# Kernel optimization log

Hardware: AMD Instinct MI355X
Metric: run time of the kernel (lower is better)

## Reference

```python
import jax, jax.numpy as jnp
import numpy as np

SEQ, B, H, OUT = 128, 256, 1024, 128


def _linear_params(key, out_dim, in_dim):
    kw, kb = jax.random.split(key)
    bound = 1.0 / np.sqrt(in_dim)
    W = jax.random.uniform(kw, (out_dim, in_dim), jnp.float32, -bound, bound)
    b = jax.random.uniform(kb, (out_dim,), jnp.float32, -bound, bound)
    return W, b


def setup_inputs() -> dict:
    key = jax.random.key(0)
    keys = jax.random.split(key, 10)
    x = jax.random.normal(keys[0], (SEQ, B), jnp.float32)
    Wfx, bfx = _linear_params(keys[1], H, 1)
    Wfh, bfh = _linear_params(keys[2], H, H)
    Wix, bix = _linear_params(keys[3], H, 1)
    Wih, bih = _linear_params(keys[4], H, H)
    Wgx, bgx = _linear_params(keys[5], H, 1)
    Wgh, bgh = _linear_params(keys[6], H, H)
    Wox, box = _linear_params(keys[7], H, 1)
    Woh, boh = _linear_params(keys[8], H, H)
    Wph, bph = _linear_params(keys[9], OUT, H)
    return dict(x=x, Wfx=Wfx, bfx=bfx, Wfh=Wfh, bfh=bfh,
                Wix=Wix, bix=bix, Wih=Wih, bih=bih,
                Wgx=Wgx, bgx=bgx, Wgh=Wgh, bgh=bgh,
                Wox=Wox, box=box, Woh=Woh, boh=boh,
                Wph=Wph, bph=bph)


def reference(x, Wfx, bfx, Wfh, bfh, Wix, bix, Wih, bih,
              Wgx, bgx, Wgh, bgh, Wox, box, Woh, boh, Wph, bph):
    # Fuse the 8 per-gate linears into two GEMMs per step (x-proj and h-proj),
    # gate order: f, i, g, o.
    Wx = jnp.concatenate([Wfx, Wix, Wgx, Wox], axis=0)      # (4H, 1)
    bx = jnp.concatenate([bfx, bix, bgx, box], axis=0)       # (4H,)
    Wh = jnp.concatenate([Wfh, Wih, Wgh, Woh], axis=0)       # (4H, H)
    bh = jnp.concatenate([bfh, bih, bgh, boh], axis=0)       # (4H,)
    Hdim = Wfh.shape[0]
    Bsz = x.shape[1]

    # x projection has input_dim=1: precompute for all timesteps at once.
    zx_all = x[:, :, None] * Wx[:, 0][None, None, :] + bx     # (S, B, 4H)

    def step(carry, zx):
        h, c = carry
        z = zx + h @ Wh.T + bh                                # (B, 4H)
        f = jax.nn.sigmoid(z[:, 0 * Hdim:1 * Hdim])
        i = jax.nn.sigmoid(z[:, 1 * Hdim:2 * Hdim])
        g = jnp.tanh(z[:, 2 * Hdim:3 * Hdim])
        o = jax.nn.sigmoid(z[:, 3 * Hdim:4 * Hdim])
        c = g * i + c * f
        h = jnp.tanh(c) * o
        return (h, c), None

    h0 = jnp.zeros((Bsz, Hdim), x.dtype)
    c0 = jnp.zeros((Bsz, Hdim), x.dtype)
    (h, c), _ = jax.lax.scan(step, (h0, c0), zx_all)
    logits = h @ Wph.T + bph                                  # (B, OUT)
    return jax.nn.softmax(logits, axis=-1)
```

## Files before the change

kernel.cpp:

```cpp
#include <hip/hip_runtime.h>
#include <hip/hip_fp16.h>
#include <cstdint>
#include <cstddef>

#define SEQ   128
#define BATCH 256
#define HDIM  1024
#define ODIM  128
#define NBLK  256

typedef _Float16 half_t;
typedef _Float16 half8 __attribute__((ext_vector_type(8)));
typedef float    f32x4 __attribute__((ext_vector_type(4)));
typedef unsigned long long u64;

#define LDS_P_OFF    131072
#define LDS_HS_OFF   (LDS_P_OFF + 2 * 64 * 36 * 4)
#define LDS_BYTES    (LDS_HS_OFF + 64 * 16 * 2)

#define HBUF_BYTES   524288
#define FLAGS_OFF    ((size_t)129 * HBUF_BYTES)

__device__ __forceinline__ float sigmoidf_(float z) {
    return 1.0f / (1.0f + __expf(-z));
}
__device__ __forceinline__ float tanhf_(float z) {
    z = fminf(fmaxf(z, -30.0f), 30.0f);
    float e = __expf(2.0f * z);
    return (e - 1.0f) / (e + 1.0f);
}

__global__ __launch_bounds__(256) void lstm_init(int* __restrict__ flags) {
    flags[blockIdx.x * 256 + threadIdx.x] = 0;
}

__global__ __launch_bounds__(512, 2) void lstm_persist(
    const float* __restrict__ x,
    const float* __restrict__ Wfh, const float* __restrict__ Wih,
    const float* __restrict__ Wgh, const float* __restrict__ Woh,
    const float* __restrict__ Wfx, const float* __restrict__ Wix,
    const float* __restrict__ Wgx, const float* __restrict__ Wox,
    const float* __restrict__ bfx, const float* __restrict__ bix,
    const float* __restrict__ bgx, const float* __restrict__ box,
    const float* __restrict__ bfh, const float* __restrict__ bih,
    const float* __restrict__ bgh, const float* __restrict__ boh,
    const float* __restrict__ Wph, const float* __restrict__ bph,
    char* __restrict__ wsbase, float* __restrict__ out)
{
    extern __shared__ char smem[];
    half_t* Bs = (half_t*)smem;
    float*  P  = (float*)(smem + LDS_P_OFF);
    half_t* Hs = (half_t*)(smem + LDS_HS_OFF);
    int* counters = (int*)(wsbase + FLAGS_OFF);

    const int tid  = threadIdx.x;
    const int blk  = blockIdx.x;
    const int grp  = blk & 3;
    const int by   = blk >> 2;
    const int m0   = grp << 6;
    const int u0   = by << 4;

    const int w    = tid >> 6;
    const int lane = tid & 63;
    const int l15  = lane & 15;
    const int q    = lane >> 4;
    const int kh   = w >> 2;
    const int mh   = w & 3;

    {
        const float* Wh[4] = {Wfh, Wih, Wgh, Woh};
        for (int d = tid; d < 8192; d += 512) {
            const int ul = d & 15, qq = (d >> 4) & 3, g = (d >> 6) & 3;
            const int kk = (d >> 8) & 15, kh2 = d >> 12;
            const float* src = Wh[g] + (size_t)(u0 + ul) * HDIM
                             + kh2 * 512 + kk * 32 + qq * 8;
            const float4 v0 = *(const float4*)src;
            const float4 v1 = *(const float4*)(src + 4);
            half8 hv;
            hv[0] = (half_t)v0.x; hv[1] = (half_t)v0.y;
            hv[2] = (half_t)v0.z; hv[3] = (half_t)v0.w;
            hv[4] = (half_t)v1.x; hv[5] = (half_t)v1.y;
            hv[6] = (half_t)v1.z; hv[7] = (half_t)v1.w;
            *(half8*)(Bs + (size_t)d * 8) = hv;
        }
    }

    const int u = u0 + l15;
    const float bf = bfx[u] + bfh[u], bi = bix[u] + bih[u];
    const float bg = bgx[u] + bgh[u], bo = box[u] + boh[u];
    const float wf = Wfx[u], wi = Wix[u], wg = Wgx[u], wo = Wox[u];

    f32x4 creg = {0.f, 0.f, 0.f, 0.f};

    __syncthreads();

    for (int t = 0; t < SEQ; ++t) {
        const half_t* hin  = (const half_t*)(wsbase + (size_t)t * HBUF_BYTES);
        half_t*       hout = (half_t*)(wsbase + (size_t)(t + 1) * HBUF_BYTES);

        f32x4 acc[4] = {};

        if (t > 0) {
            const half_t* abase = hin + (size_t)(m0 + 16 * mh + l15) * HDIM
                                + kh * 512 + q * 8;
            half8 a[16];
#pragma unroll
            for (int kk = 0; kk < 16; ++kk)
                a[kk] = *(const half8*)(abase + kk * 32);
#pragma unroll
            for (int kk = 0; kk < 16; ++kk) {
                half8 bb[4];
#pragma unroll
                for (int g = 0; g < 4; ++g)
                    bb[g] = *(const half8*)(Bs +
                        ((size_t)((kh << 12) + (kk << 8) + (g << 6) + (q << 4) + l15)) * 8);
#pragma unroll
                for (int g = 0; g < 4; ++g)
                    acc[g] = __builtin_amdgcn_mfma_f32_16x16x32_f16(
                        a[kk], bb[g], acc[g], 0, 0, 0);
            }
        }

        if (kh == 1) {
#pragma unroll
            for (int g = 0; g < 4; ++g)
                *(f32x4*)&P[(size_t)((mh >> 1) * 64 + (g << 4) + l15) * 36
                            + (mh & 1) * 16 + (q << 2)] = acc[g];
        }
        __syncthreads();

        if (kh == 0) {
            const int lr0 = (mh << 4) + (q << 2);
            const float4 xv = *(const float4*)&x[t * BATCH + m0 + lr0];
            const int pb = ((mh >> 1) * 64 + l15) * 36 + (mh & 1) * 16 + (q << 2);
            f32x4 zf = acc[0] + *(const f32x4*)&P[pb];
            f32x4 zi = acc[1] + *(const f32x4*)&P[pb + 16 * 36];
            f32x4 zg = acc[2] + *(const f32x4*)&P[pb + 32 * 36];
            f32x4 zo = acc[3] + *(const f32x4*)&P[pb + 48 * 36];
#pragma unroll
            for (int e = 0; e < 4; ++e) {
                const float xe = (e == 0) ? xv.x : (e == 1) ? xv.y
                               : (e == 2) ? xv.z : xv.w;
                const float fg = sigmoidf_(zf[e] + xe * wf + bf);
                const float ig = sigmoidf_(zi[e] + xe * wi + bi);
                const float gg = tanhf_  (zg[e] + xe * wg + bg);
                const float og = sigmoidf_(zo[e] + xe * wo + bo);
                const float cn = gg * ig + creg[e] * fg;
                creg[e] = cn;
                Hs[(lr0 + e) * 16 + l15] = (half_t)(tanhf_(cn) * og);
            }
        }
        __syncthreads();

        if (tid < 256) {
            const int lr = tid >> 2, p = tid & 3;
            const u64 v = *(const u64*)&Hs[lr * 16 + p * 4];
            u64* dst = (u64*)(hout + (size_t)(m0 + lr) * HDIM + u0 + p * 4);
            __hip_atomic_store(dst, v, __ATOMIC_RELAXED, __HIP_MEMORY_SCOPE_AGENT);
        }
        asm volatile("s_waitcnt vmcnt(0)" ::: "memory");
        __syncthreads();

        int* cnt = &counters[(size_t)((t << 2) + grp) << 6];
        if (tid == 0)
            __hip_atomic_fetch_add(cnt, 1, __ATOMIC_RELAXED,
                                   __HIP_MEMORY_SCOPE_AGENT);
        if (w == 0) {
            for (;;) {
                const int v = __hip_atomic_load(cnt, __ATOMIC_RELAXED,
                                                __HIP_MEMORY_SCOPE_AGENT);
                if (v == 64) break;
                __builtin_amdgcn_s_sleep(2);
            }
        }
        asm volatile("" ::: "memory");
        __syncthreads();
    }

    const int row = (grp << 6) + by;
    float* sm     = (float*)smem;
    float* hrow   = sm;
    float* psum   = sm + 1024;
    float* logits = sm + 1536;
    const half_t* hf = (const half_t*)(wsbase + (size_t)SEQ * HBUF_BYTES)
                     + ((size_t)row << 10);

    for (int k = tid; k < HDIM; k += 512) hrow[k] = (float)hf[k];
    __syncthreads();

    const int j = tid & 127, qt = tid >> 7;
    const float4* wp = (const float4*)(Wph + (size_t)j * HDIM + qt * 256);
    const float4* hp = (const float4*)(hrow + qt * 256);
    float s = 0.0f;
#pragma unroll 8
    for (int k4 = 0; k4 < 64; ++k4) {
        const float4 wv = wp[k4];
        const float4 hv = hp[k4];
        s += wv.x * hv.x + wv.y * hv.y + wv.z * hv.z + wv.w * hv.w;
    }
    psum[tid] = s;
    __syncthreads();
    if (tid < ODIM)
        logits[tid] = psum[tid] + psum[tid + 128] + psum[tid + 256]
                    + psum[tid + 384] + bph[tid];
    __syncthreads();
    if (tid < ODIM) {
        float mx = -1e30f;
        for (int i = 0; i < ODIM; ++i) mx = fmaxf(mx, logits[i]);
        psum[tid] = __expf(logits[tid] - mx);
    }
    __syncthreads();
    if (tid < ODIM) {
        float ssum = 0.0f;
        for (int i = 0; i < ODIM; ++i) ssum += psum[i];
        out[row * ODIM + tid] = psum[tid] / ssum;
    }
}

extern "C" void kernel_launch(void* const* d_in, const int* in_sizes, int n_in,
                              void* d_out, int out_size, void* d_ws, size_t ws_size,
                              hipStream_t stream) {
    const float* x   = (const float*)d_in[0];
    const float* Wfx = (const float*)d_in[1];
    const float* bfx = (const float*)d_in[2];
    const float* Wfh = (const float*)d_in[3];
    const float* bfh = (const float*)d_in[4];
    const float* Wix = (const float*)d_in[5];
    const float* bix = (const float*)d_in[6];
    const float* Wih = (const float*)d_in[7];
    const float* bih = (const float*)d_in[8];
    const float* Wgx = (const float*)d_in[9];
    const float* bgx = (const float*)d_in[10];
    const float* Wgh = (const float*)d_in[11];
    const float* bgh = (const float*)d_in[12];
    const float* Wox = (const float*)d_in[13];
    const float* box = (const float*)d_in[14];
    const float* Woh = (const float*)d_in[15];
    const float* boh = (const float*)d_in[16];
    const float* Wph = (const float*)d_in[17];
    const float* bph = (const float*)d_in[18];
    float* outp = (float*)d_out;

    char* ws = (char*)d_ws;
    int* flags = (int*)(ws + FLAGS_OFF);

    lstm_init<<<128, 256, 0, stream>>>(flags);

    (void)hipFuncSetAttribute((const void*)lstm_persist,
                              hipFuncAttributeMaxDynamicSharedMemorySize,
                              LDS_BYTES);

    void* args[] = {
        (void*)&x,
        (void*)&Wfh, (void*)&Wih, (void*)&Wgh, (void*)&Woh,
        (void*)&Wfx, (void*)&Wix, (void*)&Wgx, (void*)&Wox,
        (void*)&bfx, (void*)&bix, (void*)&bgx, (void*)&box,
        (void*)&bfh, (void*)&bih, (void*)&bgh, (void*)&boh,
        (void*)&Wph, (void*)&bph,
        (void*)&ws, (void*)&outp
    };
    (void)hipLaunchCooperativeKernel((const void*)lstm_persist,
                                     dim3(NBLK), dim3(512),
                                     args, LDS_BYTES, stream);
}
```

Before: 996.5 us.

## Split per-step group barrier into per-K-quarter counters waited before loads

```diff
diff --git a/kernel.cpp b/kernel.cpp
--- a/kernel.cpp
+++ b/kernel.cpp
@@ -101,12 +101,39 @@
         f32x4 acc[4] = {};
 
         if (t > 0) {
+            int* cbase = &counters[(size_t)((((t - 1) << 2) + grp) << 2) << 4];
             const half_t* abase = hin + (size_t)(m0 + 16 * mh + l15) * HDIM
                                 + kh * 512 + q * 8;
             half8 a[16];
-#pragma unroll
-            for (int kk = 0; kk < 16; ++kk)
+
+            {
+                int* c = cbase + ((kh << 1) + 0) * 16;
+                for (;;) {
+                    const int v = __hip_atomic_load(c, __ATOMIC_RELAXED,
+                                                    __HIP_MEMORY_SCOPE_AGENT);
+                    if (v == 16) break;
+                    __builtin_amdgcn_s_sleep(2);
+                }
+            }
+            asm volatile("" ::: "memory");
+#pragma unroll
+            for (int kk = 0; kk < 8; ++kk)
                 a[kk] = *(const half8*)(abase + kk * 32);
+
+            {
+                int* c = cbase + ((kh << 1) + 1) * 16;
+                for (;;) {
+                    const int v = __hip_atomic_load(c, __ATOMIC_RELAXED,
+                                                    __HIP_MEMORY_SCOPE_AGENT);
+                    if (v == 16) break;
+                    __builtin_amdgcn_s_sleep(2);
+                }
+            }
+            asm volatile("" ::: "memory");
+#pragma unroll
+            for (int kk = 8; kk < 16; ++kk)
+                a[kk] = *(const half8*)(abase + kk * 32);
+
 #pragma unroll
             for (int kk = 0; kk < 16; ++kk) {
                 half8 bb[4];
@@ -161,21 +188,24 @@
         asm volatile("s_waitcnt vmcnt(0)" ::: "memory");
         __syncthreads();
 
-        int* cnt = &counters[(size_t)((t << 2) + grp) << 6];
         if (tid == 0)
-            __hip_atomic_fetch_add(cnt, 1, __ATOMIC_RELAXED,
-                                   __HIP_MEMORY_SCOPE_AGENT);
-        if (w == 0) {
-            for (;;) {
-                const int v = __hip_atomic_load(cnt, __ATOMIC_RELAXED,
-                                                __HIP_MEMORY_SCOPE_AGENT);
-                if (v == 64) break;
-                __builtin_amdgcn_s_sleep(2);
-            }
-        }
-        asm volatile("" ::: "memory");
-        __syncthreads();
-    }
+            __hip_atomic_fetch_add(
+                &counters[(size_t)(((((t << 2) + grp) << 2) + (by >> 4))) << 4],
+                1, __ATOMIC_RELAXED, __HIP_MEMORY_SCOPE_AGENT);
+    }
+
+    if (w == 0) {
+        const int* c = &counters[(size_t)(((127 << 2) + grp) << 2) << 4];
+        for (;;) {
+            const int v = __hip_atomic_load(c + (lane & 3) * 16,
+                                            __ATOMIC_RELAXED,
+                                            __HIP_MEMORY_SCOPE_AGENT);
+            if (__all(v == 16)) break;
+            __builtin_amdgcn_s_sleep(2);
+        }
+    }
+    asm volatile("" ::: "memory");
+    __syncthreads();
 
     const int row = (grp << 6) + by;
     float* sm     = (float*)smem;
```

Measured after the change: 1.132 ms. 13.6% more time.

## Replace per-step block barrier with per-warp-row counters and wait-on-consume

Applied to the files above, without the earlier changes.

```diff
diff --git a/kernel.cpp b/kernel.cpp
--- a/kernel.cpp
+++ b/kernel.cpp
@@ -101,6 +101,13 @@
         f32x4 acc[4] = {};
 
         if (t > 0) {
+            int* c = &counters[(size_t)((((t - 1) << 2) + grp) << 2) + mh << 0];
+            c = &counters[((((size_t)(t - 1) << 2) + grp) * 4 + mh) * 16];
+            while (__hip_atomic_load(c, __ATOMIC_RELAXED,
+                                     __HIP_MEMORY_SCOPE_AGENT) != 64)
+                __builtin_amdgcn_s_sleep(2);
+            asm volatile("" ::: "memory");
+
             const half_t* abase = hin + (size_t)(m0 + 16 * mh + l15) * HDIM
                                 + kh * 512 + q * 8;
             half8 a[16];
@@ -129,14 +136,19 @@
         }
         __syncthreads();
 
+        f32x4 zf, zi, zg, zo;
+        if (kh == 0) {
+            const int pb = ((mh >> 1) * 64 + l15) * 36 + (mh & 1) * 16 + (q << 2);
+            zf = acc[0] + *(const f32x4*)&P[pb];
+            zi = acc[1] + *(const f32x4*)&P[pb + 16 * 36];
+            zg = acc[2] + *(const f32x4*)&P[pb + 32 * 36];
+            zo = acc[3] + *(const f32x4*)&P[pb + 48 * 36];
+        }
+        __syncthreads();
+
         if (kh == 0) {
             const int lr0 = (mh << 4) + (q << 2);
             const float4 xv = *(const float4*)&x[t * BATCH + m0 + lr0];
-            const int pb = ((mh >> 1) * 64 + l15) * 36 + (mh & 1) * 16 + (q << 2);
-            f32x4 zf = acc[0] + *(const f32x4*)&P[pb];
-            f32x4 zi = acc[1] + *(const f32x4*)&P[pb + 16 * 36];
-            f32x4 zg = acc[2] + *(const f32x4*)&P[pb + 32 * 36];
-            f32x4 zo = acc[3] + *(const f32x4*)&P[pb + 48 * 36];
 #pragma unroll
             for (int e = 0; e < 4; ++e) {
                 const float xe = (e == 0) ? xv.x : (e == 1) ? xv.y
@@ -149,33 +161,30 @@
                 creg[e] = cn;
                 Hs[(lr0 + e) * 16 + l15] = (half_t)(tanhf_(cn) * og);
             }
-        }
-        __syncthreads();
-
-        if (tid < 256) {
-            const int lr = tid >> 2, p = tid & 3;
+            asm volatile("s_waitcnt lgkmcnt(0)" ::: "memory");
+
+            const int lr = (mh << 4) + (lane >> 2), p = lane & 3;
             const u64 v = *(const u64*)&Hs[lr * 16 + p * 4];
             u64* dst = (u64*)(hout + (size_t)(m0 + lr) * HDIM + u0 + p * 4);
             __hip_atomic_store(dst, v, __ATOMIC_RELAXED, __HIP_MEMORY_SCOPE_AGENT);
-        }
-        asm volatile("s_waitcnt vmcnt(0)" ::: "memory");
-        __syncthreads();
-
-        int* cnt = &counters[(size_t)((t << 2) + grp) << 6];
-        if (tid == 0)
-            __hip_atomic_fetch_add(cnt, 1, __ATOMIC_RELAXED,
-                                   __HIP_MEMORY_SCOPE_AGENT);
-        if (w == 0) {
-            for (;;) {
-                const int v = __hip_atomic_load(cnt, __ATOMIC_RELAXED,
-                                                __HIP_MEMORY_SCOPE_AGENT);
-                if (v == 64) break;
-                __builtin_amdgcn_s_sleep(2);
-            }
-        }
-        asm volatile("" ::: "memory");
-        __syncthreads();
-    }
+            asm volatile("s_waitcnt vmcnt(0)" ::: "memory");
+
+            if (lane == 0)
+                __hip_atomic_fetch_add(
+                    &counters[((((size_t)t << 2) + grp) * 4 + mh) * 16],
+                    1, __ATOMIC_RELAXED, __HIP_MEMORY_SCOPE_AGENT);
+        }
+    }
+
+    {
+        int* c = &counters[(((size_t)(SEQ - 1) << 2) + grp) * 4 * 16
+                           + (size_t)(by >> 4) * 16];
+        while (__hip_atomic_load(c, __ATOMIC_RELAXED,
+                                 __HIP_MEMORY_SCOPE_AGENT) != 64)
+            __builtin_amdgcn_s_sleep(2);
+    }
+    asm volatile("" ::: "memory");
+    __syncthreads();
 
     const int row = (grp << 6) + by;
     float* sm     = (float*)smem;
```

Result: slower. 1.732 ms (+73.8%).
